# Kernel optimization log

Hardware: AMD Instinct MI355X
Metric: run time of the kernel (lower is better)

## Reference

```python
import jax, jax.numpy as jnp
import numpy as np

N_NODES = 50000
N_EDGES = 500000
H_DIM = 128
BN_EPS = 1e-5


def setup_inputs() -> dict:
    key = jax.random.key(0)
    k1, k2, k3, k4 = jax.random.split(key, 4)
    ent_emb = jax.random.normal(k1, (N_NODES, H_DIM), dtype=jnp.float32)
    neigh_w = jax.random.normal(k2, (H_DIM, H_DIM), dtype=jnp.float32) * 0.05
    gamma = jnp.ones((H_DIM,), dtype=jnp.float32)
    beta = jnp.zeros((H_DIM,), dtype=jnp.float32)
    src = jax.random.randint(k3, (N_EDGES,), 0, N_NODES, dtype=jnp.int32)
    dst = jax.random.randint(k4, (N_EDGES,), 0, N_NODES, dtype=jnp.int32)
    return {"ent_emb": ent_emb, "neigh_w": neigh_w, "gamma": gamma,
            "beta": beta, "src": src, "dst": dst}


def reference(ent_emb, neigh_w, gamma, beta, src, dst):
    # u_dot_v: per-edge dot product of src and dst node embeddings -> [E]
    e_src = ent_emb[src]                      # [E, D] gather
    scores = jnp.sum(e_src * ent_emb[dst], axis=-1)  # [E]

    # edge_softmax: softmax over incoming edges of each destination node
    seg_max = jax.ops.segment_max(scores, dst, num_segments=N_NODES)
    seg_max = jnp.where(jnp.isfinite(seg_max), seg_max, 0.0)  # empty nodes
    ex = jnp.exp(scores - seg_max[dst])
    denom = jax.ops.segment_sum(ex, dst, num_segments=N_NODES)
    norm = ex / denom[dst]                    # [E]

    # u_mul_e + sum: weighted scatter-sum of src embeddings into dst nodes
    neigh = jax.ops.segment_sum(e_src * norm[:, None], dst,
                                num_segments=N_NODES)  # [N, D]

    # linear + BatchNorm1d (training mode, batch stats) + tanh
    h = neigh @ neigh_w
    mu = jnp.mean(h, axis=0)
    var = jnp.var(h, axis=0)                  # biased, matches torch BN
    h = (h - mu) * jax.lax.rsqrt(var + BN_EPS) * gamma + beta
    return jnp.tanh(h)
```

## Files before the change

### kernel.cpp

```cpp
#include <hip/hip_runtime.h>
#include <hip/hip_bf16.h>
#include <math.h>

#define N_NODES 50000
#define N_EDGES 500000
#define H_DIM   128
#define BN_EPS  1e-5f
#define GEMM_GRID ((N_NODES + 31) / 32)
#define SCAN_NBLK ((N_NODES + 255) / 256)
#define RED_NBLK  64

typedef __attribute__((ext_vector_type(8))) short short8;
typedef __attribute__((ext_vector_type(4))) float floatx4;

__device__ __forceinline__ ushort f2bf(float x)
{
    unsigned u = __float_as_uint(x);
    unsigned r = (u + 0x7FFFu + ((u >> 16) & 1u)) >> 16;
    return (ushort)r;
}

__global__ __launch_bounds__(256) void hist_cvt_kernel(
    const int* __restrict__ dst, int* __restrict__ deg,
    const float* __restrict__ W, ushort* __restrict__ wt)
{
    int e = blockIdx.x * blockDim.x + threadIdx.x;
    if (e < N_EDGES) atomicAdd(&deg[dst[e]], 1);
    if (e < H_DIM * H_DIM) {
        int k = e >> 7, c = e & 127;
        wt[c * 128 + k] = f2bf(W[e]);
    }
}

__global__ __launch_bounds__(256) void scan_kernel(
    const int* __restrict__ deg,
    int* __restrict__ rowptr, int* __restrict__ cursor)
{
    __shared__ int bs[256];
    __shared__ int s[256];
    int t  = threadIdx.x;
    int wv = t >> 6;
    int ln = t & 63;

    for (int j = wv; j < SCAN_NBLK; j += 4) {
        int base = j * 256 + ln * 4;
        int ssum = 0;
        if (base + 3 < N_NODES) {
            int4 v = *(const int4*)(deg + base);
            ssum = v.x + v.y + v.z + v.w;
        } else {
            #pragma unroll
            for (int k = 0; k < 4; ++k)
                if (base + k < N_NODES) ssum += deg[base + k];
        }
        #pragma unroll
        for (int off = 32; off; off >>= 1)
            ssum += __shfl_xor(ssum, off);
        if (ln == 0) bs[j] = ssum;
    }
    __syncthreads();

    int val = (t < SCAN_NBLK) ? bs[t] : 0;
    s[t] = val;
    __syncthreads();
    for (int off = 1; off < 256; off <<= 1) {
        int u = (t >= off) ? s[t - off] : 0;
        __syncthreads();
        s[t] += u;
        __syncthreads();
    }
    int blockoff = (blockIdx.x == 0) ? 0 : s[blockIdx.x - 1];

    int i = blockIdx.x * 256 + t;
    int v = (i < N_NODES) ? deg[i] : 0;
    bs[t] = v;
    __syncthreads();
    for (int off = 1; off < 256; off <<= 1) {
        int u = (t >= off) ? bs[t - off] : 0;
        __syncthreads();
        bs[t] += u;
        __syncthreads();
    }
    int excl = bs[t] - v + blockoff;
    if (i < N_NODES) {
        rowptr[i] = excl;
        cursor[i] = excl;
        if (i == N_NODES - 1) rowptr[N_NODES] = excl + v;
    }
}

__global__ __launch_bounds__(256) void csr_scatter_kernel(
    const int* __restrict__ src, const int* __restrict__ dst,
    int* __restrict__ cursor, int* __restrict__ csr_src)
{
    int e = blockIdx.x * blockDim.x + threadIdx.x;
    if (e >= N_EDGES) return;
    int pos = atomicAdd(&cursor[dst[e]], 1);
    csr_src[pos] = src[e];
}

__global__ __launch_bounds__(256) void fused_agg_gemm_kernel(
    const float* __restrict__ emb,
    const int* __restrict__ rowptr,
    const int* __restrict__ csr_src,
    const ushort* __restrict__ wt,
    float* __restrict__ h,
    float* __restrict__ partial)
{
    __shared__ ushort A_s[32 * 128];
    __shared__ float  red_s[128 * 9];
    __shared__ float  red_q[128 * 9];

    int t  = threadIdx.x;
    int r0 = blockIdx.x * 32;

    int grp  = t >> 5;
    int lane = t & 31;

    for (int ri = 0; ri < 4; ++ri) {
        int row  = ri * 8 + grp;
        int node = r0 + row;
        float4 o = {0.f, 0.f, 0.f, 0.f};

        if (node < N_NODES) {
            int beg = rowptr[node];
            int end = rowptr[node + 1];
            const float4 b = *((const float4*)(emb + (size_t)node * H_DIM) + lane);

            float m = -INFINITY;
            float denom = 0.f;
            float4 acc = {0.f, 0.f, 0.f, 0.f};

            int e = beg;
            for (; e + 4 <= end; e += 4) {
                float4 a[4];
                float  p[4];
                #pragma unroll
                for (int u = 0; u < 4; ++u) {
                    int s = csr_src[e + u];
                    a[u] = *((const float4*)(emb + (size_t)s * H_DIM) + lane);
                }
                #pragma unroll
                for (int u = 0; u < 4; ++u)
                    p[u] = a[u].x * b.x + a[u].y * b.y + a[u].z * b.z + a[u].w * b.w;
                #pragma unroll
                for (int off = 16; off; off >>= 1) {
                    #pragma unroll
                    for (int u = 0; u < 4; ++u)
                        p[u] += __shfl_xor(p[u], off);
                }
                float mn = fmaxf(fmaxf(fmaxf(p[0], p[1]), fmaxf(p[2], p[3])), m);
                float corr = __expf(m - mn);
                float w[4];
                #pragma unroll
                for (int u = 0; u < 4; ++u) w[u] = __expf(p[u] - mn);
                denom = denom * corr + w[0] + w[1] + w[2] + w[3];
                acc.x = acc.x * corr + a[0].x*w[0] + a[1].x*w[1] + a[2].x*w[2] + a[3].x*w[3];
                acc.y = acc.y * corr + a[0].y*w[0] + a[1].y*w[1] + a[2].y*w[2] + a[3].y*w[3];
                acc.z = acc.z * corr + a[0].z*w[0] + a[1].z*w[1] + a[2].z*w[2] + a[3].z*w[3];
                acc.w = acc.w * corr + a[0].w*w[0] + a[1].w*w[1] + a[2].w*w[2] + a[3].w*w[3];
                m = mn;
            }
            for (; e < end; ++e) {
                int s = csr_src[e];
                float4 a = *((const float4*)(emb + (size_t)s * H_DIM) + lane);
                float p = a.x * b.x + a.y * b.y + a.z * b.z + a.w * b.w;
                #pragma unroll
                for (int off = 16; off; off >>= 1)
                    p += __shfl_xor(p, off);
                float mn   = fmaxf(m, p);
                float corr = __expf(m - mn);
                float w    = __expf(p - mn);
                denom = denom * corr + w;
                acc.x = acc.x * corr + a.x * w;
                acc.y = acc.y * corr + a.y * w;
                acc.z = acc.z * corr + a.z * w;
                acc.w = acc.w * corr + a.w * w;
                m = mn;
            }

            float inv = (end > beg) ? (1.0f / denom) : 0.f;
            o.x = acc.x * inv; o.y = acc.y * inv;
            o.z = acc.z * inv; o.w = acc.w * inv;
        }

        unsigned lo = (unsigned)f2bf(o.x) | ((unsigned)f2bf(o.y) << 16);
        unsigned hi = (unsigned)f2bf(o.z) | ((unsigned)f2bf(o.w) << 16);
        int col = (lane * 4) ^ ((row & 7) << 3);
        uint2 pk; pk.x = lo; pk.y = hi;
        *(uint2*)&A_s[row * 128 + col] = pk;
    }
    __syncthreads();

    int w      = t >> 6;
    int lane64 = t & 63;
    int rbase  = (w >> 1) * 16;
    int c0     = (w & 1) * 64;
    int l15    = lane64 & 15;
    int kgrp   = lane64 >> 4;
    int arow   = rbase + l15;
    int k0l    = kgrp * 8;

    floatx4 acc4[4] = {{0.f,0.f,0.f,0.f},{0.f,0.f,0.f,0.f},
                       {0.f,0.f,0.f,0.f},{0.f,0.f,0.f,0.f}};

    #pragma unroll
    for (int ks = 0; ks < 4; ++ks) {
        int k0 = ks * 32 + k0l;
        short8 af = *(const short8*)&A_s[arow * 128 + (k0 ^ ((arow & 7) << 3))];
        #pragma unroll
        for (int ct = 0; ct < 4; ++ct) {
            int col = c0 + ct * 16 + l15;
            short8 bf = *(const short8*)(wt + (size_t)col * 128 + k0);
            acc4[ct] = __builtin_amdgcn_mfma_f32_16x16x32_bf16(af, bf, acc4[ct], 0, 0, 0);
        }
    }

    int contrib = (w >> 1) * 4 + kgrp;
    #pragma unroll
    for (int ct = 0; ct < 4; ++ct) {
        int col = c0 + ct * 16 + l15;
        float ps = 0.f, pq = 0.f;
        #pragma unroll
        for (int reg = 0; reg < 4; ++reg) {
            float v = acc4[ct][reg];
            int gr = r0 + rbase + kgrp * 4 + reg;
            if (gr < N_NODES) h[(size_t)gr * H_DIM + col] = v;
            ps += v;
            pq += v * v;
        }
        red_s[col * 9 + contrib] = ps;
        red_q[col * 9 + contrib] = pq;
    }
    __syncthreads();

    float s = 0.f;
    if (t < 128) {
        #pragma unroll
        for (int q = 0; q < 8; ++q) s += red_s[t * 9 + q];
    } else if (t < 256) {
        #pragma unroll
        for (int q = 0; q < 8; ++q) s += red_q[(t - 128) * 9 + q];
    }
    partial[(size_t)blockIdx.x * 256 + t] = s;
}

__global__ __launch_bounds__(256) void reduce_partials_kernel(
    const float* __restrict__ partial, float* __restrict__ partial2)
{
    int t = threadIdx.x;
    int g = blockIdx.x;
    float s = 0.f;
    for (int b = g; b < GEMM_GRID; b += RED_NBLK)
        s += partial[(size_t)b * 256 + t];
    partial2[(size_t)g * 256 + t] = s;
}

__global__ __launch_bounds__(256) void bn_fold_tanh_kernel(
    const float* __restrict__ partial2,
    const float* __restrict__ gamma,
    const float* __restrict__ beta,
    float* __restrict__ h)
{
    __shared__ float tot[256];
    __shared__ float sc_s[128];
    __shared__ float sh_s[128];
    int t = threadIdx.x;

    float s = 0.f;
    #pragma unroll 8
    for (int b = 0; b < RED_NBLK; ++b)
        s += partial2[b * 256 + t];
    tot[t] = s;
    __syncthreads();
    if (t < 128) {
        float cs = tot[t];
        float cq = tot[t + 128];
        const float invN = 1.0f / (float)N_NODES;
        float mu  = cs * invN;
        float var = cq * invN - mu * mu;
        float sc  = gamma[t] * rsqrtf(var + BN_EPS);
        sc_s[t] = sc;
        sh_s[t] = beta[t] - mu * sc;
    }
    __syncthreads();

    const size_t total4 = (size_t)N_NODES * H_DIM / 4;
    for (size_t i = (size_t)blockIdx.x * 256 + t; i < total4;
         i += (size_t)gridDim.x * 256) {
        size_t idx4 = i * 4;
        int c = (int)(idx4 & (H_DIM - 1));
        float4 v = *(float4*)(h + idx4);
        v.x = tanhf(v.x * sc_s[c + 0] + sh_s[c + 0]);
        v.y = tanhf(v.y * sc_s[c + 1] + sh_s[c + 1]);
        v.z = tanhf(v.z * sc_s[c + 2] + sh_s[c + 2]);
        v.w = tanhf(v.w * sc_s[c + 3] + sh_s[c + 3]);
        *(float4*)(h + idx4) = v;
    }
}

extern "C" void kernel_launch(void* const* d_in, const int* in_sizes, int n_in,
                              void* d_out, int out_size, void* d_ws, size_t ws_size,
                              hipStream_t stream)
{
    const float* ent_emb = (const float*)d_in[0];
    const float* neigh_w = (const float*)d_in[1];
    const float* gamma   = (const float*)d_in[2];
    const float* beta    = (const float*)d_in[3];
    const int*   src     = (const int*)d_in[4];
    const int*   dst     = (const int*)d_in[5];
    float* out = (float*)d_out;

    int*    deg      = (int*)d_ws;
    int*    rowptr   = deg + N_NODES;
    int*    cursor   = rowptr + N_NODES + 1;
    int*    csr_src  = cursor + N_NODES;
    float*  partial  = (float*)(csr_src + N_EDGES);
    float*  partial2 = partial + (size_t)GEMM_GRID * 256;
    ushort* wt       = (ushort*)(partial2 + (size_t)RED_NBLK * 256);

    hipMemsetAsync(deg, 0, N_NODES * sizeof(int), stream);

    hist_cvt_kernel<<<(N_EDGES + 255) / 256, 256, 0, stream>>>(dst, deg, neigh_w, wt);
    scan_kernel<<<SCAN_NBLK, 256, 0, stream>>>(deg, rowptr, cursor);
    csr_scatter_kernel<<<(N_EDGES + 255) / 256, 256, 0, stream>>>(src, dst, cursor, csr_src);

    fused_agg_gemm_kernel<<<GEMM_GRID, 256, 0, stream>>>(
        ent_emb, rowptr, csr_src, wt, out, partial);

    reduce_partials_kernel<<<RED_NBLK, 256, 0, stream>>>(partial, partial2);
    bn_fold_tanh_kernel<<<512, 256, 0, stream>>>(partial2, gamma, beta, out);
}
```

Measured before the change: 172.7 us.

## Split fused aggregate+GEMM into separate kernels and split scan into two passes

Unfuses the edge-softmax aggregation from the MFMA GEMM. Aggregation now runs in its own kernel with 8 nodes per block, writing bf16 neighbour rows to a workspace buffer, and a separate GEMM+stats kernel reads them back. The single scan kernel, which had every block redundantly re-reduce all block sums, is replaced by a block-sum kernel followed by a final scan kernel. The aim is better load balance and occupancy for the irregular gather phase and less redundant scan work. The cost is an extra global round trip of the bf16 aggregate and two extra kernel launches.

```diff
diff --git a/kernel.cpp b/kernel.cpp
--- a/kernel.cpp
+++ b/kernel.cpp
@@ -32,36 +32,43 @@
     }
 }
 
-__global__ __launch_bounds__(256) void scan_kernel(
-    const int* __restrict__ deg,
+__global__ __launch_bounds__(256) void scan_partial_kernel(
+    const int* __restrict__ deg, int* __restrict__ blocksum)
+{
+    __shared__ int red[256];
+    int t = threadIdx.x;
+    int i = blockIdx.x * 256 + t;
+    red[t] = (i < N_NODES) ? deg[i] : 0;
+    __syncthreads();
+    #pragma unroll
+    for (int off = 128; off; off >>= 1) {
+        if (t < off) red[t] += red[t + off];
+        __syncthreads();
+    }
+    if (t == 0) blocksum[blockIdx.x] = red[0];
+}
+
+__global__ __launch_bounds__(256) void scan_final_kernel(
+    const int* __restrict__ deg, const int* __restrict__ blocksum,
     int* __restrict__ rowptr, int* __restrict__ cursor)
 {
     __shared__ int bs[256];
     __shared__ int s[256];
-    int t  = threadIdx.x;
-    int wv = t >> 6;
-    int ln = t & 63;
-
-    for (int j = wv; j < SCAN_NBLK; j += 4) {
-        int base = j * 256 + ln * 4;
-        int ssum = 0;
-        if (base + 3 < N_NODES) {
-            int4 v = *(const int4*)(deg + base);
-            ssum = v.x + v.y + v.z + v.w;
-        } else {
-            #pragma unroll
-            for (int k = 0; k < 4; ++k)
-                if (base + k < N_NODES) ssum += deg[base + k];
-        }
-        #pragma unroll
-        for (int off = 32; off; off >>= 1)
-            ssum += __shfl_xor(ssum, off);
-        if (ln == 0) bs[j] = ssum;
-    }
-    __syncthreads();
-
-    int val = (t < SCAN_NBLK) ? bs[t] : 0;
-    s[t] = val;
+    int t = threadIdx.x;
+
+    bs[t] = (t < SCAN_NBLK) ? blocksum[t] : 0;
+    __syncthreads();
+    for (int off = 1; off < 256; off <<= 1) {
+        int v = (t >= off) ? bs[t - off] : 0;
+        __syncthreads();
+        bs[t] += v;
+        __syncthreads();
+    }
+    int blockoff = (blockIdx.x == 0) ? 0 : bs[blockIdx.x - 1];
+
+    int i = blockIdx.x * 256 + t;
+    int v = (i < N_NODES) ? deg[i] : 0;
+    s[t] = v;
     __syncthreads();
     for (int off = 1; off < 256; off <<= 1) {
         int u = (t >= off) ? s[t - off] : 0;
@@ -69,19 +76,7 @@
         s[t] += u;
         __syncthreads();
     }
-    int blockoff = (blockIdx.x == 0) ? 0 : s[blockIdx.x - 1];
-
-    int i = blockIdx.x * 256 + t;
-    int v = (i < N_NODES) ? deg[i] : 0;
-    bs[t] = v;
-    __syncthreads();
-    for (int off = 1; off < 256; off <<= 1) {
-        int u = (t >= off) ? bs[t - off] : 0;
-        __syncthreads();
-        bs[t] += u;
-        __syncthreads();
-    }
-    int excl = bs[t] - v + blockoff;
+    int excl = s[t] - v + blockoff;
     if (i < N_NODES) {
         rowptr[i] = excl;
         cursor[i] = excl;
@@ -99,98 +94,91 @@
     csr_src[pos] = src[e];
 }
 
-__global__ __launch_bounds__(256) void fused_agg_gemm_kernel(
+__global__ __launch_bounds__(256) void node_aggregate_kernel(
     const float* __restrict__ emb,
     const int* __restrict__ rowptr,
     const int* __restrict__ csr_src,
+    ushort* __restrict__ neigh_bf)
+{
+    int node = blockIdx.x * 8 + (threadIdx.x >> 5);
+    int lane = threadIdx.x & 31;
+    if (node >= N_NODES) return;
+
+    int beg = rowptr[node];
+    int end = rowptr[node + 1];
+
+    const float4 b = *((const float4*)(emb + (size_t)node * H_DIM) + lane);
+
+    float m = -INFINITY;
+    float denom = 0.f;
+    float4 acc = {0.f, 0.f, 0.f, 0.f};
+
+    int e = beg;
+    for (; e + 4 <= end; e += 4) {
+        float4 a[4];
+        float  p[4];
+        #pragma unroll
+        for (int u = 0; u < 4; ++u) {
+            int s = csr_src[e + u];
+            a[u] = *((const float4*)(emb + (size_t)s * H_DIM) + lane);
+        }
+        #pragma unroll
+        for (int u = 0; u < 4; ++u)
+            p[u] = a[u].x * b.x + a[u].y * b.y + a[u].z * b.z + a[u].w * b.w;
+        #pragma unroll
+        for (int off = 16; off; off >>= 1) {
+            #pragma unroll
+            for (int u = 0; u < 4; ++u)
+                p[u] += __shfl_xor(p[u], off);
+        }
+        float mn = fmaxf(fmaxf(fmaxf(p[0], p[1]), fmaxf(p[2], p[3])), m);
+        float corr = __expf(m - mn);
+        float w[4];
+        #pragma unroll
+        for (int u = 0; u < 4; ++u) w[u] = __expf(p[u] - mn);
+        denom = denom * corr + w[0] + w[1] + w[2] + w[3];
+        acc.x = acc.x * corr + a[0].x*w[0] + a[1].x*w[1] + a[2].x*w[2] + a[3].x*w[3];
+        acc.y = acc.y * corr + a[0].y*w[0] + a[1].y*w[1] + a[2].y*w[2] + a[3].y*w[3];
+        acc.z = acc.z * corr + a[0].z*w[0] + a[1].z*w[1] + a[2].z*w[2] + a[3].z*w[3];
+        acc.w = acc.w * corr + a[0].w*w[0] + a[1].w*w[1] + a[2].w*w[2] + a[3].w*w[3];
+        m = mn;
+    }
+    for (; e < end; ++e) {
+        int s = csr_src[e];
+        float4 a = *((const float4*)(emb + (size_t)s * H_DIM) + lane);
+        float p = a.x * b.x + a.y * b.y + a.z * b.z + a.w * b.w;
+        #pragma unroll
+        for (int off = 16; off; off >>= 1)
+            p += __shfl_xor(p, off);
+        float mn   = fmaxf(m, p);
+        float corr = __expf(m - mn);
+        float w    = __expf(p - mn);
+        denom = denom * corr + w;
+        acc.x = acc.x * corr + a.x * w;
+        acc.y = acc.y * corr + a.y * w;
+        acc.z = acc.z * corr + a.z * w;
+        acc.w = acc.w * corr + a.w * w;
+        m = mn;
+    }
+
+    float inv = (end > beg) ? (1.0f / denom) : 0.f;
+    unsigned lo = (unsigned)f2bf(acc.x * inv) | ((unsigned)f2bf(acc.y * inv) << 16);
+    unsigned hi = (unsigned)f2bf(acc.z * inv) | ((unsigned)f2bf(acc.w * inv) << 16);
+    uint2 pk; pk.x = lo; pk.y = hi;
+    *((uint2*)(neigh_bf + (size_t)node * H_DIM) + lane) = pk;
+}
+
+__global__ __launch_bounds__(256) void gemm_stats_kernel(
+    const ushort* __restrict__ neigh_bf,
     const ushort* __restrict__ wt,
     float* __restrict__ h,
     float* __restrict__ partial)
 {
-    __shared__ ushort A_s[32 * 128];
-    __shared__ float  red_s[128 * 9];
-    __shared__ float  red_q[128 * 9];
+    __shared__ float red_s[128 * 9];
+    __shared__ float red_q[128 * 9];
 
     int t  = threadIdx.x;
     int r0 = blockIdx.x * 32;
-
-    int grp  = t >> 5;
-    int lane = t & 31;
-
-    for (int ri = 0; ri < 4; ++ri) {
-        int row  = ri * 8 + grp;
-        int node = r0 + row;
-        float4 o = {0.f, 0.f, 0.f, 0.f};
-
-        if (node < N_NODES) {
-            int beg = rowptr[node];
-            int end = rowptr[node + 1];
-            const float4 b = *((const float4*)(emb + (size_t)node * H_DIM) + lane);
-
-            float m = -INFINITY;
-            float denom = 0.f;
-            float4 acc = {0.f, 0.f, 0.f, 0.f};
-
-            int e = beg;
-            for (; e + 4 <= end; e += 4) {
-                float4 a[4];
-                float  p[4];
-                #pragma unroll
-                for (int u = 0; u < 4; ++u) {
-                    int s = csr_src[e + u];
-                    a[u] = *((const float4*)(emb + (size_t)s * H_DIM) + lane);
-                }
-                #pragma unroll
-                for (int u = 0; u < 4; ++u)
-                    p[u] = a[u].x * b.x + a[u].y * b.y + a[u].z * b.z + a[u].w * b.w;
-                #pragma unroll
-                for (int off = 16; off; off >>= 1) {
-                    #pragma unroll
-                    for (int u = 0; u < 4; ++u)
-                        p[u] += __shfl_xor(p[u], off);
-                }
-                float mn = fmaxf(fmaxf(fmaxf(p[0], p[1]), fmaxf(p[2], p[3])), m);
-                float corr = __expf(m - mn);
-                float w[4];
-                #pragma unroll
-                for (int u = 0; u < 4; ++u) w[u] = __expf(p[u] - mn);
-                denom = denom * corr + w[0] + w[1] + w[2] + w[3];
-                acc.x = acc.x * corr + a[0].x*w[0] + a[1].x*w[1] + a[2].x*w[2] + a[3].x*w[3];
-                acc.y = acc.y * corr + a[0].y*w[0] + a[1].y*w[1] + a[2].y*w[2] + a[3].y*w[3];
-                acc.z = acc.z * corr + a[0].z*w[0] + a[1].z*w[1] + a[2].z*w[2] + a[3].z*w[3];
-                acc.w = acc.w * corr + a[0].w*w[0] + a[1].w*w[1] + a[2].w*w[2] + a[3].w*w[3];
-                m = mn;
-            }
-            for (; e < end; ++e) {
-                int s = csr_src[e];
-                float4 a = *((const float4*)(emb + (size_t)s * H_DIM) + lane);
-                float p = a.x * b.x + a.y * b.y + a.z * b.z + a.w * b.w;
-                #pragma unroll
-                for (int off = 16; off; off >>= 1)
-                    p += __shfl_xor(p, off);
-                float mn   = fmaxf(m, p);
-                float corr = __expf(m - mn);
-                float w    = __expf(p - mn);
-                denom = denom * corr + w;
-                acc.x = acc.x * corr + a.x * w;
-                acc.y = acc.y * corr + a.y * w;
-                acc.z = acc.z * corr + a.z * w;
-                acc.w = acc.w * corr + a.w * w;
-                m = mn;
-            }
-
-            float inv = (end > beg) ? (1.0f / denom) : 0.f;
-            o.x = acc.x * inv; o.y = acc.y * inv;
-            o.z = acc.z * inv; o.w = acc.w * inv;
-        }
-
-        unsigned lo = (unsigned)f2bf(o.x) | ((unsigned)f2bf(o.y) << 16);
-        unsigned hi = (unsigned)f2bf(o.z) | ((unsigned)f2bf(o.w) << 16);
-        int col = (lane * 4) ^ ((row & 7) << 3);
-        uint2 pk; pk.x = lo; pk.y = hi;
-        *(uint2*)&A_s[row * 128 + col] = pk;
-    }
-    __syncthreads();
 
     int w      = t >> 6;
     int lane64 = t & 63;
@@ -198,7 +186,7 @@
     int c0     = (w & 1) * 64;
     int l15    = lane64 & 15;
     int kgrp   = lane64 >> 4;
-    int arow   = rbase + l15;
+    int grow   = r0 + rbase + l15;
     int k0l    = kgrp * 8;
 
     floatx4 acc4[4] = {{0.f,0.f,0.f,0.f},{0.f,0.f,0.f,0.f},
@@ -207,7 +195,9 @@
     #pragma unroll
     for (int ks = 0; ks < 4; ++ks) {
         int k0 = ks * 32 + k0l;
-        short8 af = *(const short8*)&A_s[arow * 128 + (k0 ^ ((arow & 7) << 3))];
+        short8 af = {0,0,0,0,0,0,0,0};
+        if (grow < N_NODES)
+            af = *(const short8*)(neigh_bf + (size_t)grow * H_DIM + k0);
         #pragma unroll
         for (int ct = 0; ct < 4; ++ct) {
             int col = c0 + ct * 16 + l15;
@@ -238,7 +228,7 @@
     if (t < 128) {
         #pragma unroll
         for (int q = 0; q < 8; ++q) s += red_s[t * 9 + q];
-    } else if (t < 256) {
+    } else {
         #pragma unroll
         for (int q = 0; q < 8; ++q) s += red_q[(t - 128) * 9 + q];
     }
@@ -315,18 +305,23 @@
     int*    rowptr   = deg + N_NODES;
     int*    cursor   = rowptr + N_NODES + 1;
     int*    csr_src  = cursor + N_NODES;
-    float*  partial  = (float*)(csr_src + N_EDGES);
+    int*    blocksum = csr_src + N_EDGES;
+    float*  partial  = (float*)(blocksum + SCAN_NBLK);
     float*  partial2 = partial + (size_t)GEMM_GRID * 256;
     ushort* wt       = (ushort*)(partial2 + (size_t)RED_NBLK * 256);
+    ushort* neigh_bf = wt + H_DIM * H_DIM;
 
     hipMemsetAsync(deg, 0, N_NODES * sizeof(int), stream);
 
     hist_cvt_kernel<<<(N_EDGES + 255) / 256, 256, 0, stream>>>(dst, deg, neigh_w, wt);
-    scan_kernel<<<SCAN_NBLK, 256, 0, stream>>>(deg, rowptr, cursor);
+    scan_partial_kernel<<<SCAN_NBLK, 256, 0, stream>>>(deg, blocksum);
+    scan_final_kernel<<<SCAN_NBLK, 256, 0, stream>>>(deg, blocksum, rowptr, cursor);
     csr_scatter_kernel<<<(N_EDGES + 255) / 256, 256, 0, stream>>>(src, dst, cursor, csr_src);
 
-    fused_agg_gemm_kernel<<<GEMM_GRID, 256, 0, stream>>>(
-        ent_emb, rowptr, csr_src, wt, out, partial);
+    node_aggregate_kernel<<<(N_NODES + 7) / 8, 256, 0, stream>>>(
+        ent_emb, rowptr, csr_src, neigh_bf);
+
+    gemm_stats_kernel<<<GEMM_GRID, 256, 0, stream>>>(neigh_bf, wt, out, partial);
 
     reduce_partials_kernel<<<RED_NBLK, 256, 0, stream>>>(partial, partial2);
     bn_fold_tanh_kernel<<<512, 256, 0, stream>>>(partial2, gamma, beta, out);
```

Measured after the change: 150.6 us. -12.8%, faster.
